# Optimization experiments

Hardware: AMD Instinct MI355X
Metric: run time of the kernel (lower is better)

The kernel has to match this reference:

```python
import jax, jax.numpy as jnp
import numpy as np

EPS = 1e-6  # LayerNorm epsilon


def setup_inputs() -> dict:
    key = jax.random.key(0)
    ks = jax.random.split(key, 12)
    B, S, T, E = 8, 2048, 2048, 512
    sc = 1.0 / np.sqrt(E)
    inp = {
        "encoder_outputs": jax.random.normal(ks[0], (B, S, E), jnp.float32),
        "emotion": jax.random.normal(ks[1], (B, T, E), jnp.float32),
        "mask": jax.random.randint(ks[2], (B, S, T), 0, 2).astype(bool),
        "Wq": jax.random.normal(ks[3], (E, E), jnp.float32) * sc,
        "bq": jnp.zeros((E,), jnp.float32),
        "Wk": jax.random.normal(ks[4], (E, E), jnp.float32) * sc,
        "bk": jnp.zeros((E,), jnp.float32),
        "Wv": jax.random.normal(ks[5], (E, E), jnp.float32) * sc,
        "bv": jnp.zeros((E,), jnp.float32),
        "Wo": jax.random.normal(ks[6], (E, E), jnp.float32) * sc,
        "gamma": jnp.ones((E,), jnp.float32),
        "beta": jnp.zeros((E,), jnp.float32),
    }
    return inp


def reference(encoder_outputs, emotion, mask, Wq, bq, Wk, bk, Wv, bv, Wo, gamma, beta):
    # Linear projections (torch Linear: x @ W.T + b)
    q = encoder_outputs @ Wq.T + bq          # [B,S,E]
    k = emotion @ Wk.T + bk                  # [B,T,E]
    v = emotion @ Wv.T + bv                  # [B,T,E]
    logits = jnp.einsum("bse,bte->bst", q, k)  # [B,S,T]
    logits = jnp.where(mask, jnp.float32(-1e18), logits)
    weights = jax.nn.softmax(logits, axis=-1)   # dropout1 = identity (eval)
    contexts = jnp.einsum("bst,bte->bse", weights, v)
    attn = contexts @ Wo.T                   # output_linear, no bias
    attn = encoder_outputs + attn            # dropout2 = identity (eval)
    # LayerNorm (std-based, as in common hand-rolled LayerNorm)
    mean = attn.mean(-1, keepdims=True)
    std = attn.std(-1, keepdims=True)
    context = gamma * (attn - mean) / (std + EPS) + beta
    context = encoder_outputs + context      # dropout3 = identity (eval)
    return context
```

## Files before the change

### kernel.cpp

```cpp
#include <hip/hip_runtime.h>
#include <math.h>
#include <stdint.h>


#define BB 8
#define SS 2048
#define TT 2048
#define EE 512

typedef __attribute__((ext_vector_type(8))) short short8;
typedef __attribute__((ext_vector_type(4))) short short4v;
typedef __attribute__((ext_vector_type(4))) float f32x4;

__device__ __forceinline__ uint16_t f2bf(float f) {
  uint32_t u = __builtin_bit_cast(uint32_t, f);
  u += 0x7fffu + ((u >> 16) & 1u);
  return (uint16_t)(u >> 16);
}
__device__ __forceinline__ float bf2f(uint16_t h) {
  uint32_t u = ((uint32_t)h) << 16;
  return __builtin_bit_cast(float, u);
}

__device__ __forceinline__ size_t toff(int row, int col, int ld) {
  return (size_t)(row >> 4) * ((size_t)ld << 4) + ((size_t)(col >> 3) << 7)
       + ((row & 15) << 3) + (col & 7);
}

__device__ __forceinline__ void gld16(const void* g, void* l) {
  __builtin_amdgcn_global_load_lds(
      (const __attribute__((address_space(1))) void*)g,
      (__attribute__((address_space(3))) void*)l, 16, 0, 0);
}

template<int ASRC, int BSRC, int EPI, int WN>
__global__ __launch_bounds__(256, 2) void mgemm(
    const void* __restrict__ Ap, const void* __restrict__ Alo,
    const void* __restrict__ Bp, const void* __restrict__ Blo,
    void* __restrict__ Cp, void* __restrict__ C2,
    const float* __restrict__ bias, const float* __restrict__ bias2,
    const float* __restrict__ resid,
    const int* __restrict__ mask, float* __restrict__ sZ,
    int K, int lda, int ldb, int ldc,
    size_t sA, size_t sB, size_t sC, size_t sM)
{
  constexpr bool ALOARR = (ASRC == 0);
  constexpr bool BLOARR = (BSRC == 0);
  constexpr bool T3     = (ASRC == 0) && (BSRC == 0);
  constexpr bool T2     = (ASRC == 0) && (BSRC == 1);
  constexpr int  BN     = 32 * WN;
  constexpr int  ABYTES = ALOARR ? 16384 : 8192;
  constexpr int  BBYTES = BLOARR ? BN * 128 : BN * 64;

  __shared__ char smem[ABYTES + BBYTES];

  const int tid  = threadIdx.x;
  const int lane = tid & 63, wv = tid >> 6;
  const int z    = blockIdx.z;
  const int bm   = blockIdx.y * 128;
  const int bn   = blockIdx.x * BN;
  const int fr   = lane & 15;
  const int wm   = (wv & 1) * 64;
  const int wn   = (wv >> 1) * (16 * WN);

  const f32x4 zero = {0.f, 0.f, 0.f, 0.f};
  f32x4 acc[4][WN];
#pragma unroll
  for (int i = 0; i < 4; ++i)
#pragma unroll
    for (int j = 0; j < WN; ++j) acc[i][j] = zero;

  const size_t loff = (size_t)lane * 8;
  const uint16_t* gAh = (const uint16_t*)Ap + sA * z + (size_t)(bm >> 4) * 16 * lda + loff;
  const uint16_t* gAl = ALOARR ? (const uint16_t*)Alo + sA * z + (size_t)(bm >> 4) * 16 * lda + loff : nullptr;
  const uint16_t* gBh = (const uint16_t*)Bp + sB * z + (size_t)(bn >> 4) * 16 * ldb + loff;
  const uint16_t* gBl = BLOARR ? (const uint16_t*)Blo + sB * z + (size_t)(bn >> 4) * 16 * ldb + loff : nullptr;

  for (int k0 = 0; k0 < K; k0 += 32) {
    const size_t ka = (size_t)k0 * 16;
    __syncthreads();
#pragma unroll
    for (int t = 0; t < 2; ++t) { int s = wv + t * 4;
      gld16(gAh + (size_t)s * 16 * lda + ka, &smem[s * 1024]); }
    if constexpr (ALOARR) {
#pragma unroll
      for (int t = 0; t < 2; ++t) { int s = wv + t * 4;
        gld16(gAl + (size_t)s * 16 * lda + ka, &smem[8192 + s * 1024]); }
    }
#pragma unroll
    for (int t = 0; t < WN / 2; ++t) { int s = wv + t * 4;
      gld16(gBh + (size_t)s * 16 * ldb + ka, &smem[ABYTES + s * 1024]); }
    if constexpr (BLOARR) {
#pragma unroll
      for (int t = 0; t < WN / 2; ++t) { int s = wv + t * 4;
        gld16(gBl + (size_t)s * 16 * ldb + ka, &smem[ABYTES + BN * 64 + s * 1024]); }
    }
    __syncthreads();

    short8 ah[4], bh[WN], al_[4], bl_[WN];
#pragma unroll
    for (int i = 0; i < 4; ++i) {
      const char* p = smem + ((wm >> 4) + i) * 1024 + (lane << 4);
      ah[i] = *(const short8*)p;
      if constexpr (ALOARR) al_[i] = *(const short8*)(p + 8192);
    }
#pragma unroll
    for (int j = 0; j < WN; ++j) {
      const char* p = smem + ABYTES + ((wn >> 4) + j) * 1024 + (lane << 4);
      bh[j] = *(const short8*)p;
      if constexpr (BLOARR) bl_[j] = *(const short8*)(p + BN * 64);
    }
#pragma unroll
    for (int i = 0; i < 4; ++i)
#pragma unroll
      for (int j = 0; j < WN; ++j) {
        acc[i][j] = __builtin_amdgcn_mfma_f32_16x16x32_bf16(ah[i], bh[j], acc[i][j], 0, 0, 0);
        if constexpr (T3) {
          acc[i][j] = __builtin_amdgcn_mfma_f32_16x16x32_bf16(ah[i], bl_[j], acc[i][j], 0, 0, 0);
          acc[i][j] = __builtin_amdgcn_mfma_f32_16x16x32_bf16(al_[i], bh[j], acc[i][j], 0, 0, 0);
        } else if constexpr (T2) {
          acc[i][j] = __builtin_amdgcn_mfma_f32_16x16x32_bf16(al_[i], bh[j], acc[i][j], 0, 0, 0);
        }
      }
  }

  if constexpr (EPI == 5) {
    const unsigned long long* __restrict__ mb = (const unsigned long long*)mask;
    const int c0 = bn + wn;
    const int sh = ((c0 & 255) >> 2) + (fr >> 2);
    const size_t mbase = (size_t)z * 65536 + (size_t)((c0 >> 8) << 2) + (fr & 3);
    unsigned long long mw[4][4];
#pragma unroll
    for (int i = 0; i < 4; ++i)
#pragma unroll
      for (int g = 0; g < 4; ++g) {
        const int row = bm + wm + i * 16 + (lane >> 4) * 4 + g;
        mw[i][g] = mb[mbase + (size_t)row * 32];
      }
#pragma unroll
    for (int i = 0; i < 4; ++i) {
      const int row0 = bm + wm + i * 16 + (lane >> 4) * 4;
#pragma unroll
      for (int g = 0; g < 4; ++g) {
        const int row = row0 + g;
        float rs = 0.f;
#pragma unroll
        for (int j = 0; j < WN; ++j) {
          const int col = bn + wn + j * 16 + fr;
          const bool msk = (mw[i][g] >> (sh + j * 4)) & 1ull;
          const float e = msk ? 0.f : __expf(acc[i][j][g] - 60.0f);
          ((uint16_t*)Cp)[sC * z + toff(row, col, ldc)] = f2bf(e);
          rs += e;
        }
        rs += __shfl_xor(rs, 1);
        rs += __shfl_xor(rs, 2);
        rs += __shfl_xor(rs, 4);
        rs += __shfl_xor(rs, 8);
        if ((lane & 15) == 0) atomicAdd(&sZ[(size_t)z * SS + row], rs);
      }
    }
  } else {
#pragma unroll
    for (int i = 0; i < 4; ++i) {
      const int row0 = bm + wm + i * 16 + (lane >> 4) * 4;
#pragma unroll
      for (int g = 0; g < 4; ++g) {
        const int row = row0 + g;
        float invZ = 1.0f;
        if constexpr (EPI == 6) invZ = 1.0f / sZ[(size_t)z * SS + row];
#pragma unroll
        for (int j = 0; j < WN; ++j) {
          const int col = bn + wn + j * 16 + fr;
          float v = acc[i][j][g];
          if constexpr (EPI == 0) {
            const float* bp = (z == 0) ? bias : bias2;
            const size_t ci = sC * z + toff(row, col, ldc);
            v += bp[col];
            uint16_t h = f2bf(v);
            ((uint16_t*)Cp)[ci] = h;
            if (z == 0) ((uint16_t*)C2)[ci] = f2bf(v - bf2f(h));
          } else if constexpr (EPI == 1) {
            v += bias[row];
            ((uint16_t*)Cp)[sC * z + toff(row, col, ldc)] = f2bf(v);
          } else if constexpr (EPI == 4) {
            v += resid[(size_t)row * ldc + col];
            ((float*)Cp)[sC * z + (size_t)row * ldc + col] = v;
          } else {
            ((uint16_t*)Cp)[sC * z + toff(row, col, ldc)] = f2bf(v * invZ);
          }
        }
      }
    }
  }
}

__device__ __forceinline__ void split_core(
    const float* __restrict__ x, uint16_t* __restrict__ hi,
    uint16_t* __restrict__ lo, int bid)
{
  __shared__ uint16_t lh[256 * 8 + 16 * 8];
  __shared__ uint16_t ll[256 * 8 + 16 * 8];
  const int t   = threadIdx.x;
  const int seg = bid >> 2, q = bid & 3;

  const float* src = x + (size_t)(seg * 16 + (t >> 4)) * 512 + q * 128 + (t & 15) * 8;
  float4 a = *(const float4*)src;
  float4 b = *(const float4*)(src + 4);
  float v[8] = {a.x, a.y, a.z, a.w, b.x, b.y, b.z, b.w};

  const int slot = (t & 15) * 16 + (t >> 4);
  uint16_t* ph = lh + slot * 8 + (slot >> 4) * 8;
  uint16_t* pl = ll + slot * 8 + (slot >> 4) * 8;
#pragma unroll
  for (int e = 0; e < 8; ++e) {
    uint16_t h = f2bf(v[e]);
    ph[e] = h;
    pl[e] = f2bf(v[e] - bf2f(h));
  }
  __syncthreads();

  const uint16_t* qh = lh + t * 8 + (t >> 4) * 8;
  const uint16_t* ql = ll + t * 8 + (t >> 4) * 8;
  const size_t off = (size_t)seg * 8192 + (size_t)(q * 16 + (t >> 4)) * 128 + (t & 15) * 8;
  *(short8*)(hi + off) = *(const short8*)qh;
  *(short8*)(lo + off) = *(const short8*)ql;
}

__global__ __launch_bounds__(256) void prepass(
    const float* __restrict__ enc, const float* __restrict__ emo,
    uint16_t* __restrict__ hi, uint16_t* __restrict__ lo, size_t stride,
    const int* __restrict__ mask, unsigned long long* __restrict__ mbits)
{
  const int t    = threadIdx.x;
  const int lane = t & 63, wv = t >> 6;
  const int arr  = blockIdx.x >> 10;
  const int lb   = blockIdx.x & 1023;

  const float* src = (arr ? emo : enc);
  float4 f[8];
#pragma unroll
  for (int r = 0; r < 8; ++r)
    f[r] = *((const float4*)src + (size_t)lb * 2048 + r * 256 + t);

  const int4* mp = (const int4*)mask + (size_t)blockIdx.x * 4096;
  int4 m[16];
#pragma unroll
  for (int r = 0; r < 16; ++r)
    m[r] = mp[r * 256 + t];

  uint16_t* hp = hi + (size_t)arr * stride;
  uint16_t* lp = lo + (size_t)arr * stride;
#pragma unroll
  for (int r = 0; r < 8; ++r) {
    const int lf  = lb * 2048 + r * 256 + t;
    const int row = lf >> 7;
    const int k   = (lf & 127) * 4;
    const size_t off = (size_t)(row >> 4) * 8192 + (size_t)(k >> 3) * 128
                     + (row & 15) * 8 + (k & 7);
    const float v[4] = {f[r].x, f[r].y, f[r].z, f[r].w};
    short4v hv, lv;
#pragma unroll
    for (int e = 0; e < 4; ++e) {
      const uint16_t h = f2bf(v[e]);
      hv[e] = (short)h;
      lv[e] = (short)f2bf(v[e] - bf2f(h));
    }
    *(short4v*)(hp + off) = hv;
    *(short4v*)(lp + off) = lv;
  }

#pragma unroll
  for (int r = 0; r < 16; ++r) {
    const unsigned long long b0 = __ballot(m[r].x != 0);
    const unsigned long long b1 = __ballot(m[r].y != 0);
    const unsigned long long b2 = __ballot(m[r].z != 0);
    const unsigned long long b3 = __ballot(m[r].w != 0);
    if (lane < 4) {
      const unsigned long long w = (lane == 0) ? b0 : (lane == 1) ? b1
                                 : (lane == 2) ? b2 : b3;
      mbits[(size_t)blockIdx.x * 256 + r * 16 + wv * 4 + lane] = w;
    }
  }
}

__global__ __launch_bounds__(256) void split_w4(
    const float* __restrict__ x0, const float* __restrict__ x1,
    const float* __restrict__ x2, const float* __restrict__ x3,
    uint16_t* __restrict__ hi0, uint16_t* __restrict__ lo0, size_t stride)
{
  const int w   = blockIdx.x >> 7;
  const int bid = blockIdx.x & 127;
  const float* x = (w == 0) ? x0 : (w == 1) ? x1 : (w == 2) ? x2 : x3;
  split_core(x, hi0 + w * stride, lo0 + w * stride, bid);
}

__global__ __launch_bounds__(256) void ln_kernel(
    const float* __restrict__ X, const float* __restrict__ enc,
    const float* __restrict__ gamma, const float* __restrict__ beta,
    float* __restrict__ out)
{
  const int row = blockIdx.x * 4 + (threadIdx.x >> 6);
  const int lane = threadIdx.x & 63;
  const size_t base = (size_t)row * EE;
  const int o0 = lane * 4, o1 = 256 + lane * 4;

  float4 x0 = *(const float4*)(X + base + o0);
  float4 x1 = *(const float4*)(X + base + o1);
  float s = x0.x + x0.y + x0.z + x0.w + x1.x + x1.y + x1.z + x1.w;
#pragma unroll
  for (int off = 32; off > 0; off >>= 1) s += __shfl_xor(s, off);
  const float mean = s * (1.0f / 512.0f);

  float d[8] = {x0.x - mean, x0.y - mean, x0.z - mean, x0.w - mean,
                x1.x - mean, x1.y - mean, x1.z - mean, x1.w - mean};
  float s2 = 0.f;
#pragma unroll
  for (int i = 0; i < 8; ++i) s2 = fmaf(d[i], d[i], s2);
#pragma unroll
  for (int off = 32; off > 0; off >>= 1) s2 += __shfl_xor(s2, off);
  const float stdv = sqrtf(s2 * (1.0f / 512.0f));
  const float inv = 1.0f / (stdv + 1e-6f);

  float4 g0 = *(const float4*)(gamma + o0);
  float4 g1 = *(const float4*)(gamma + o1);
  float4 b0 = *(const float4*)(beta + o0);
  float4 b1 = *(const float4*)(beta + o1);
  float4 e0 = *(const float4*)(enc + base + o0);
  float4 e1 = *(const float4*)(enc + base + o1);

  float4 r0, r1;
  r0.x = e0.x + g0.x * d[0] * inv + b0.x;
  r0.y = e0.y + g0.y * d[1] * inv + b0.y;
  r0.z = e0.z + g0.z * d[2] * inv + b0.z;
  r0.w = e0.w + g0.w * d[3] * inv + b0.w;
  r1.x = e1.x + g1.x * d[4] * inv + b1.x;
  r1.y = e1.y + g1.y * d[5] * inv + b1.y;
  r1.z = e1.z + g1.z * d[6] * inv + b1.z;
  r1.w = e1.w + g1.w * d[7] * inv + b1.w;
  *(float4*)(out + base + o0) = r0;
  *(float4*)(out + base + o1) = r1;
}

extern "C" void kernel_launch(void* const* d_in, const int* in_sizes, int n_in,
                              void* d_out, int out_size, void* d_ws, size_t ws_size,
                              hipStream_t stream) {
  const float* enc   = (const float*)d_in[0];
  const float* emo   = (const float*)d_in[1];
  const int*   mask  = (const int*)d_in[2];
  const float* Wq    = (const float*)d_in[3];
  const float* bq    = (const float*)d_in[4];
  const float* Wk    = (const float*)d_in[5];
  const float* bk    = (const float*)d_in[6];
  const float* Wv    = (const float*)d_in[7];
  const float* bv    = (const float*)d_in[8];
  const float* Wo    = (const float*)d_in[9];
  const float* gamma = (const float*)d_in[10];
  const float* beta  = (const float*)d_in[11];
  float* out = (float*)d_out;
  char*  ws  = (char*)d_ws;

  const size_t SZ = (size_t)BB * SS * EE;
  size_t off = 0;
  uint16_t* enc_h = (uint16_t*)(ws + off); off += SZ * 2;
  uint16_t* enc_l = (uint16_t*)(ws + off); off += SZ * 2;
  uint16_t* emo_h = (uint16_t*)(ws + off); off += SZ * 2;
  uint16_t* emo_l = (uint16_t*)(ws + off); off += SZ * 2;
  uint16_t* q_hi  = (uint16_t*)(ws + off); off += SZ * 2;
  uint16_t* q_lo  = (uint16_t*)(ws + off); off += SZ * 2;
  uint16_t* k_hi  = (uint16_t*)(ws + off); off += SZ * 2;
  uint16_t* k_lo  = (uint16_t*)(ws + off); off += SZ * 2;
  uint16_t* vT    = (uint16_t*)(ws + off); off += SZ * 2;
  uint16_t* ctx   = (uint16_t*)(ws + off); off += SZ * 2;
  uint16_t* wq_h  = (uint16_t*)(ws + off); off += EE * EE * 2;
  uint16_t* wq_l  = (uint16_t*)(ws + off); off += EE * EE * 2;
  uint16_t* wk_h  = (uint16_t*)(ws + off); off += EE * EE * 2;
  uint16_t* wk_l  = (uint16_t*)(ws + off); off += EE * EE * 2;
  uint16_t* wv_h  = (uint16_t*)(ws + off); off += EE * EE * 2;
  uint16_t* wv_l  = (uint16_t*)(ws + off); off += EE * EE * 2;
  uint16_t* wo_h  = (uint16_t*)(ws + off); off += EE * EE * 2;
  uint16_t* wo_l  = (uint16_t*)(ws + off); off += EE * EE * 2;
  uint16_t* P_u   = (uint16_t*)(ws + off); off += (size_t)BB * SS * TT * 2;
  float*    sZ    = (float*)(ws + off);    off += (size_t)BB * SS * 4;
  (void)wk_l; (void)wv_l; (void)wo_l;

  unsigned long long* mbits = (unsigned long long*)k_lo;

  const dim3 blk(256);

  split_w4<<<dim3(512), blk, 0, stream>>>(Wq, Wk, Wv, Wo, wq_h, wq_l,
                                          (size_t)2 * EE * EE);
  prepass<<<dim3(2048), blk, 0, stream>>>(enc, emo, enc_h, enc_l,
                                          (size_t)2 * SZ, mask, mbits);
  hipMemsetAsync(sZ, 0, (size_t)BB * SS * 4, stream);

  mgemm<0, 0, 0, 4><<<dim3(4, 128, 2), blk, 0, stream>>>(
      enc_h, enc_l, wq_h, wq_l, q_hi, q_lo, bq, bk, nullptr, nullptr, nullptr,
      EE, EE, EE, EE, 2 * SZ, (size_t)2 * EE * EE, 2 * SZ, 0);
  mgemm<1, 1, 1, 4><<<dim3(128, 4, 1), blk, 0, stream>>>(
      wv_h, nullptr, emo_h, nullptr, vT, nullptr, bv, nullptr, nullptr,
      nullptr, nullptr, EE, EE, EE, BB * TT, 0, 0, 0, 0);

  mgemm<0, 1, 5, 4><<<dim3(16, 16, 8), blk, 0, stream>>>(
      q_hi, q_lo, k_hi, nullptr, P_u, nullptr, nullptr, nullptr, nullptr,
      (const int*)mbits, sZ, EE, EE, EE, TT,
      (size_t)SS * EE, (size_t)TT * EE, (size_t)SS * TT, 0);

  mgemm<1, 1, 6, 4><<<dim3(4, 16, 8), blk, 0, stream>>>(
      P_u, nullptr, vT, nullptr, ctx, nullptr, nullptr, nullptr, nullptr,
      nullptr, sZ, TT, TT, BB * TT, EE,
      (size_t)SS * TT, (size_t)TT * 16, (size_t)SS * EE, 0);

  mgemm<1, 1, 4, 4><<<dim3(4, 128, 1), blk, 0, stream>>>(
      ctx, nullptr, wo_h, nullptr, out, nullptr, nullptr, nullptr, enc,
      nullptr, nullptr, EE, EE, EE, EE, 0, 0, 0, 0);
  ln_kernel<<<dim3(BB * SS / 4), blk, 0, stream>>>(out, enc, gamma, beta, out);
}
```

Baseline: 556.9 us.

## Fuse mask bit-packing into the QK^T GEMM via shared memory

Removes mask ballot-packing from the prepass kernel and instead has each QK^T tile block load its own 128x128 int mask tile at kernel start, pack it with ballots into a shared-memory bitmask, and read it in the exp epilogue. This drops the global write and re-read of the packed mask buffer. The prepass gets lighter, but the mask loads now sit at the front of the GEMM and the mask tile is read per block rather than once per element. The shared bitmask also uses a different bit layout, so the shift indexing is changed to match.

```diff
diff --git a/kernel.cpp b/kernel.cpp
--- a/kernel.cpp
+++ b/kernel.cpp
@@ -53,6 +53,7 @@
   constexpr int  BBYTES = BLOARR ? BN * 128 : BN * 64;
 
   __shared__ char smem[ABYTES + BBYTES];
+  __shared__ unsigned long long pm[(EPI == 5) ? 256 : 1];
 
   const int tid  = threadIdx.x;
   const int lane = tid & 63, wv = tid >> 6;
@@ -62,6 +63,27 @@
   const int fr   = lane & 15;
   const int wm   = (wv & 1) * 64;
   const int wn   = (wv >> 1) * (16 * WN);
+
+  if constexpr (EPI == 5) {
+    const int* mz = mask + sM * z;
+    int4 mm[16];
+#pragma unroll
+    for (int r = 0; r < 16; ++r)
+      mm[r] = *(const int4*)(mz + (size_t)(bm + r * 8 + (tid >> 5)) * ldc
+                                + bn + (tid & 31) * 4);
+#pragma unroll
+    for (int r = 0; r < 16; ++r) {
+      const unsigned long long b0 = __ballot(mm[r].x != 0);
+      const unsigned long long b1 = __ballot(mm[r].y != 0);
+      const unsigned long long b2 = __ballot(mm[r].z != 0);
+      const unsigned long long b3 = __ballot(mm[r].w != 0);
+      if (lane < 4) {
+        const unsigned long long w64 = (lane == 0) ? b0 : (lane == 1) ? b1
+                                     : (lane == 2) ? b2 : b3;
+        pm[(r * 4 + wv) * 4 + lane] = w64;
+      }
+    }
+  }
 
   const f32x4 zero = {0.f, 0.f, 0.f, 0.f};
   f32x4 acc[4][WN];
@@ -125,17 +147,14 @@
   }
 
   if constexpr (EPI == 5) {
-    const unsigned long long* __restrict__ mb = (const unsigned long long*)mask;
-    const int c0 = bn + wn;
-    const int sh = ((c0 & 255) >> 2) + (fr >> 2);
-    const size_t mbase = (size_t)z * 65536 + (size_t)((c0 >> 8) << 2) + (fr & 3);
+    const int sh0 = (wn >> 6) * 16 + (fr >> 2);
     unsigned long long mw[4][4];
 #pragma unroll
     for (int i = 0; i < 4; ++i)
 #pragma unroll
       for (int g = 0; g < 4; ++g) {
-        const int row = bm + wm + i * 16 + (lane >> 4) * 4 + g;
-        mw[i][g] = mb[mbase + (size_t)row * 32];
+        const int lrow = wm + i * 16 + (lane >> 4) * 4 + g;
+        mw[i][g] = pm[(lrow >> 1) * 4 + (fr & 3)];
       }
 #pragma unroll
     for (int i = 0; i < 4; ++i) {
@@ -143,6 +162,7 @@
 #pragma unroll
       for (int g = 0; g < 4; ++g) {
         const int row = row0 + g;
+        const int sh  = sh0 + (g & 1) * 32;
         float rs = 0.f;
 #pragma unroll
         for (int j = 0; j < WN; ++j) {
@@ -228,11 +248,9 @@
 
 __global__ __launch_bounds__(256) void prepass(
     const float* __restrict__ enc, const float* __restrict__ emo,
-    uint16_t* __restrict__ hi, uint16_t* __restrict__ lo, size_t stride,
-    const int* __restrict__ mask, unsigned long long* __restrict__ mbits)
+    uint16_t* __restrict__ hi, uint16_t* __restrict__ lo, size_t stride)
 {
   const int t    = threadIdx.x;
-  const int lane = t & 63, wv = t >> 6;
   const int arr  = blockIdx.x >> 10;
   const int lb   = blockIdx.x & 1023;
 
@@ -241,12 +259,6 @@
 #pragma unroll
   for (int r = 0; r < 8; ++r)
     f[r] = *((const float4*)src + (size_t)lb * 2048 + r * 256 + t);
-
-  const int4* mp = (const int4*)mask + (size_t)blockIdx.x * 4096;
-  int4 m[16];
-#pragma unroll
-  for (int r = 0; r < 16; ++r)
-    m[r] = mp[r * 256 + t];
 
   uint16_t* hp = hi + (size_t)arr * stride;
   uint16_t* lp = lo + (size_t)arr * stride;
@@ -267,19 +279,6 @@
     }
     *(short4v*)(hp + off) = hv;
     *(short4v*)(lp + off) = lv;
-  }
-
-#pragma unroll
-  for (int r = 0; r < 16; ++r) {
-    const unsigned long long b0 = __ballot(m[r].x != 0);
-    const unsigned long long b1 = __ballot(m[r].y != 0);
-    const unsigned long long b2 = __ballot(m[r].z != 0);
-    const unsigned long long b3 = __ballot(m[r].w != 0);
-    if (lane < 4) {
-      const unsigned long long w = (lane == 0) ? b0 : (lane == 1) ? b1
-                                 : (lane == 2) ? b2 : b3;
-      mbits[(size_t)blockIdx.x * 256 + r * 16 + wv * 4 + lane] = w;
-    }
   }
 }
 
@@ -381,16 +380,14 @@
   uint16_t* wo_l  = (uint16_t*)(ws + off); off += EE * EE * 2;
   uint16_t* P_u   = (uint16_t*)(ws + off); off += (size_t)BB * SS * TT * 2;
   float*    sZ    = (float*)(ws + off);    off += (size_t)BB * SS * 4;
-  (void)wk_l; (void)wv_l; (void)wo_l;
-
-  unsigned long long* mbits = (unsigned long long*)k_lo;
+  (void)k_lo; (void)wk_l; (void)wv_l; (void)wo_l;
 
   const dim3 blk(256);
 
   split_w4<<<dim3(512), blk, 0, stream>>>(Wq, Wk, Wv, Wo, wq_h, wq_l,
                                           (size_t)2 * EE * EE);
   prepass<<<dim3(2048), blk, 0, stream>>>(enc, emo, enc_h, enc_l,
-                                          (size_t)2 * SZ, mask, mbits);
+                                          (size_t)2 * SZ);
   hipMemsetAsync(sZ, 0, (size_t)BB * SS * 4, stream);
 
   mgemm<0, 0, 0, 4><<<dim3(4, 128, 2), blk, 0, stream>>>(
@@ -402,8 +399,8 @@
 
   mgemm<0, 1, 5, 4><<<dim3(16, 16, 8), blk, 0, stream>>>(
       q_hi, q_lo, k_hi, nullptr, P_u, nullptr, nullptr, nullptr, nullptr,
-      (const int*)mbits, sZ, EE, EE, EE, TT,
-      (size_t)SS * EE, (size_t)TT * EE, (size_t)SS * TT, 0);
+      mask, sZ, EE, EE, EE, TT,
+      (size_t)SS * EE, (size_t)TT * EE, (size_t)SS * TT, (size_t)SS * TT);
 
   mgemm<1, 1, 6, 4><<<dim3(4, 16, 8), blk, 0, stream>>>(
       P_u, nullptr, vT, nullptr, ctx, nullptr, nullptr, nullptr, nullptr,
```

New measurement: 541.6 us. -2.7%, faster.
